# Optimization experiments

Hardware: AMD Instinct MI355X
Metric: run time of the kernel (lower is better)

The kernel has to match this reference:

```python
import jax, jax.numpy as jnp
import numpy as np

B, S, D, H = 4, 1024, 1024, 16
DK = D // H  # 64


def setup_inputs() -> dict:
    key = jax.random.key(0)
    kx, kq, kk, kv, ko = jax.random.split(key, 5)
    scale = 1.0 / np.sqrt(D)
    x = jax.random.normal(kx, (B, S, D), dtype=jnp.float32)
    # per-head torch nn.Linear weights stacked: [H, d_k, d_model]
    Wq = jax.random.uniform(kq, (H, DK, D), jnp.float32, -scale, scale)
    Wk = jax.random.uniform(kk, (H, DK, D), jnp.float32, -scale, scale)
    Wv = jax.random.uniform(kv, (H, DK, D), jnp.float32, -scale, scale)
    Wo = jax.random.uniform(ko, (D, D), jnp.float32, -scale, scale)  # torch layout [out, in]
    # causal mask, broadcastable to (B, H, S, S); True = keep
    mask = jnp.tril(jnp.ones((S, S), dtype=bool))[None, None]
    return {"x": x, "Wq": Wq, "Wk": Wk, "Wv": Wv, "Wo": Wo, "mask": mask}


def reference(x, Wq, Wk, Wv, Wo, mask):
    # self-attention: context = x. Batched equivalent of the per-head loop.
    Q = jnp.einsum('bsd,hkd->bhsk', x, Wq)  # (B,H,S,DK)
    K = jnp.einsum('bsd,hkd->bhsk', x, Wk)
    V = jnp.einsum('bsd,hkd->bhsk', x, Wv)
    scores = jnp.einsum('bhqd,bhkd->bhqk', Q, K) / jnp.sqrt(jnp.float32(DK))
    scores = jnp.where(mask, scores, jnp.float32(-jnp.inf))
    weights = jax.nn.softmax(scores, axis=-1)  # (B,H,S,S)
    out = jnp.einsum('bhqk,bhkd->bhqd', weights, V)  # (B,H,S,DK)
    # concat heads along feature dim (head order preserved), then W_o
    concat = jnp.swapaxes(out, 1, 2).reshape(B, S, D)
    output = jnp.einsum('bqd,od->bqo', concat, Wo)
    return output, weights
```

## Files before the change

kernel.cpp:

```cpp
#include <hip/hip_runtime.h>
#include <hip/hip_bf16.h>

#define BB 4
#define SS 1024
#define DD 1024
#define HH 16
#define DKK 64

typedef __bf16 bf16;
typedef __bf16 bf16x8 __attribute__((ext_vector_type(8)));
typedef __bf16 bf16x4 __attribute__((ext_vector_type(4)));
typedef float f32x4 __attribute__((ext_vector_type(4)));

#define MFMA(a, b, c) __builtin_amdgcn_mfma_f32_16x16x32_bf16((a), (b), (c), 0, 0, 0)

__device__ __forceinline__ bf16x8 load8(const bf16* p) {
    return *reinterpret_cast<const bf16x8*>(p);
}

__device__ __forceinline__ void gload16(const bf16* g, bf16* l) {
    __builtin_amdgcn_global_load_lds(
        (const __attribute__((address_space(1))) void*)g,
        (__attribute__((address_space(3))) void*)l, 16, 0, 0);
}

__global__ __launch_bounds__(256) void cvt_bf16(const float* __restrict__ x,
                                                const float* __restrict__ Wq,
                                                const float* __restrict__ Wk,
                                                const float* __restrict__ Wv,
                                                const float* __restrict__ Wo,
                                                bf16* __restrict__ dst) {
    const size_t MEG = 1024 * 1024;
    size_t e = ((size_t)blockIdx.x * 256 + threadIdx.x) * 4;
    const float* src;
    size_t off;
    if (e < 4 * MEG)      { src = x;  off = e; }
    else if (e < 5 * MEG) { src = Wq; off = e - 4 * MEG; }
    else if (e < 6 * MEG) { src = Wk; off = e - 5 * MEG; }
    else if (e < 7 * MEG) { src = Wv; off = e - 6 * MEG; }
    else                  { src = Wo; off = e - 7 * MEG; }
    f32x4 v = *reinterpret_cast<const f32x4*>(src + off);
    bf16x4 o;
    o[0] = (bf16)v[0]; o[1] = (bf16)v[1]; o[2] = (bf16)v[2]; o[3] = (bf16)v[3];
    *reinterpret_cast<bf16x4*>(dst + e) = o;
}

template <int MODE>
__global__ __launch_bounds__(256) void gemm128(const bf16* __restrict__ A,
                                               const bf16* __restrict__ Bm,
                                               void* __restrict__ o0,
                                               void* __restrict__ o1,
                                               void* __restrict__ o2,
                                               float* __restrict__ Wgt) {
    const int lane = threadIdx.x & 63;
    const int wave = threadIdx.x >> 6;
    const int wr = wave >> 1, wc = wave & 1;
    const int m0 = blockIdx.x * 128;
    const int n0 = blockIdx.y * 128;
    const int K = DD;

    __shared__ __align__(16) bf16 As[128][32];
    __shared__ __align__(16) bf16 Bs[128][32];

    const int r0 = wave * 32 + (lane >> 2);
    const int r1 = r0 + 16;
    const int csw = ((lane & 3) ^ (r0 & 3)) * 8;

    const bf16* Ag0 = A + (size_t)(m0 + r0) * K + csw;
    const bf16* Ag1 = A + (size_t)(m0 + r1) * K + csw;
    const bf16* Bg0 = Bm + (size_t)(n0 + r0) * K + csw;
    const bf16* Bg1 = Bm + (size_t)(n0 + r1) * K + csw;
    bf16* Aw0 = &As[wave * 32][0];
    bf16* Aw1 = &As[wave * 32 + 16][0];
    bf16* Bw0 = &Bs[wave * 32][0];
    bf16* Bw1 = &Bs[wave * 32 + 16][0];

    const int rsw = ((lane >> 4) ^ (lane & 3)) * 8;
    const int rrow = lane & 15;

    f32x4 acc[4][4] = {};

    for (int k0 = 0; k0 < K; k0 += 32) {
        __syncthreads();
        gload16(Ag0 + k0, Aw0);
        gload16(Ag1 + k0, Aw1);
        gload16(Bg0 + k0, Bw0);
        gload16(Bg1 + k0, Bw1);
        __syncthreads();
        bf16x8 af[4], bfr[4];
#pragma unroll
        for (int i = 0; i < 4; i++)
            af[i] = *reinterpret_cast<const bf16x8*>(&As[wr * 64 + i * 16 + rrow][rsw]);
#pragma unroll
        for (int j = 0; j < 4; j++)
            bfr[j] = *reinterpret_cast<const bf16x8*>(&Bs[wc * 64 + j * 16 + rrow][rsw]);
#pragma unroll
        for (int i = 0; i < 4; i++)
#pragma unroll
            for (int j = 0; j < 4; j++)
                acc[i][j] = MFMA(af[i], bfr[j], acc[i][j]);
    }

    if constexpr (MODE == 0) {
        bf16* Qo = (bf16*)o0;
        bf16* Ko = (bf16*)o1;
        bf16* Vto = (bf16*)o2;
        const int z = n0 >> 10;
#pragma unroll
        for (int i = 0; i < 4; i++)
#pragma unroll
            for (int j = 0; j < 4; j++)
#pragma unroll
                for (int r = 0; r < 4; r++) {
                    int m = m0 + wr * 64 + i * 16 + (lane >> 4) * 4 + r;
                    int n = n0 + wc * 64 + j * 16 + (lane & 15);
                    int b = m >> 10, s = m & 1023;
                    int nn = n & 1023, h = nn >> 6, dk = nn & 63;
                    bf16 v = (bf16)acc[i][j][r];
                    if (z == 0)
                        Qo[(((size_t)(b * HH + h)) * SS + s) * DKK + dk] = v;
                    else if (z == 1)
                        Ko[(((size_t)(b * HH + h)) * SS + s) * DKK + dk] = v;
                    else
                        Vto[(((size_t)(b * HH + h)) * DKK + dk) * SS + s] = v;
                }
        const int bid = blockIdx.y * 32 + blockIdx.x;
        const int zrow = threadIdx.x >> 2;
        const int zcl = threadIdx.x & 3;
        const f32x4 z4 = {0.f, 0.f, 0.f, 0.f};
        for (int band = bid; band < 1024; band += 768) {
            const int bh = band >> 4, qb = band & 15;
            const int c0 = (qb + 1) * 64;
            const int nc4 = (1024 - c0) >> 2;
            if (nc4 <= 0) continue;
            float* rp = Wgt + ((size_t)bh * SS + qb * 64 + zrow) * SS + c0;
            for (int c = zcl; c < nc4; c += 4)
                *reinterpret_cast<f32x4*>(rp + c * 4) = z4;
        }
    } else {
        float* Out = (float*)o0;
#pragma unroll
        for (int i = 0; i < 4; i++)
#pragma unroll
            for (int j = 0; j < 4; j++)
#pragma unroll
                for (int r = 0; r < 4; r++) {
                    int m = m0 + wr * 64 + i * 16 + (lane >> 4) * 4 + r;
                    int n = n0 + wc * 64 + j * 16 + (lane & 15);
                    Out[(size_t)m * DD + n] = acc[i][j][r];
                }
    }
}

__global__ __launch_bounds__(256, 4) void attn(const bf16* __restrict__ Q,
                                               const bf16* __restrict__ K,
                                               const bf16* __restrict__ Vt,
                                               float* __restrict__ Wgt,
                                               bf16* __restrict__ Ctx) {
    const int tid = threadIdx.x;
    const int lane = tid & 63;
    const int wave = tid >> 6;
    const int bh = blockIdx.x;
    const int qb = (blockIdx.y + (blockIdx.x & 3)) & 15;
    const int q0 = qb * 64 + wave * 16;
    const int lr = lane & 15;
    const int g = lane >> 4;
    const int lk8 = g * 8;
    const int rbase = g * 4;
    const int own_diag = q0 >> 4;
    const int nch = qb + 1;

    const bf16* Qb = Q + (size_t)bh * SS * DKK;
    const bf16* Kb = K + (size_t)bh * SS * DKK;
    const bf16* Vb = Vt + (size_t)bh * DKK * SS;
    float* Wrow = Wgt + ((size_t)bh * SS + q0) * SS;

    __shared__ __align__(16) bf16 Ks[2][64][64];
    __shared__ __align__(16) bf16 Vs[2][64][64];
    __shared__ __align__(16) bf16 Ps[4][16][40];

    const int skr = tid >> 2;
    const int sc0 = tid & 3;
    const int sw0 = (sc0 ^ (skr & 7)) * 8;
    const int sw1 = ((sc0 + 4) ^ (skr & 7)) * 8;

    bf16x8 qa0 = load8(Qb + (size_t)(q0 + lr) * DKK + lk8);
    bf16x8 qa1 = load8(Qb + (size_t)(q0 + lr) * DKK + 32 + lk8);
#pragma unroll
    for (int i = 0; i < 8; i++) {
        qa0[i] = (bf16)((float)qa0[i] * 0.125f);
        qa1[i] = (bf16)((float)qa1[i] * 0.125f);
    }

    const int rsw0 = (g ^ (lr & 7)) * 8;
    const int rsw1 = ((4 + g) ^ (lr & 7)) * 8;

    float sl[4] = {0.f, 0.f, 0.f, 0.f};

    {
        bf16x8 ka = load8(Kb + (size_t)skr * DKK + sc0 * 8);
        bf16x8 kb_ = load8(Kb + (size_t)skr * DKK + (sc0 + 4) * 8);
        *reinterpret_cast<bf16x8*>(&Ks[0][skr][sw0]) = ka;
        *reinterpret_cast<bf16x8*>(&Ks[0][skr][sw1]) = kb_;
        __syncthreads();
        for (int ch = 0; ch < nch; ch++) {
            const int cur = ch & 1;
            if (ch + 1 < nch) {
                ka = load8(Kb + (size_t)((ch + 1) * 64 + skr) * DKK + sc0 * 8);
                kb_ = load8(Kb + (size_t)((ch + 1) * 64 + skr) * DKK + (sc0 + 4) * 8);
            }
#pragma unroll
            for (int t = 0; t < 4; t++) {
                const int kt = ch * 4 + t;
                if (kt <= own_diag) {
                    bf16x8 kb0 = *reinterpret_cast<const bf16x8*>(&Ks[cur][t * 16 + lr][rsw0]);
                    bf16x8 kb1 = *reinterpret_cast<const bf16x8*>(&Ks[cur][t * 16 + lr][rsw1]);
                    f32x4 sc = {};
                    sc = MFMA(qa0, kb0, sc);
                    sc = MFMA(qa1, kb1, sc);
                    const int kcol = kt * 16 + lr;
#pragma unroll
                    for (int r = 0; r < 4; r++)
                        sl[r] += (kcol <= q0 + rbase + r) ? __expf(sc[r]) : 0.f;
                }
            }
            if (ch + 1 < nch) {
                *reinterpret_cast<bf16x8*>(&Ks[cur ^ 1][skr][sw0]) = ka;
                *reinterpret_cast<bf16x8*>(&Ks[cur ^ 1][skr][sw1]) = kb_;
            }
            __syncthreads();
        }
    }
    float inv[4];
#pragma unroll
    for (int r = 0; r < 4; r++) {
        float t = sl[r];
        t += __shfl_xor(t, 1);
        t += __shfl_xor(t, 2);
        t += __shfl_xor(t, 4);
        t += __shfl_xor(t, 8);
        inv[r] = 1.f / t;
    }

    f32x4 oacc[4] = {};
    {
        bf16x8 ka = load8(Kb + (size_t)skr * DKK + sc0 * 8);
        bf16x8 kb_ = load8(Kb + (size_t)skr * DKK + (sc0 + 4) * 8);
        bf16x8 va = load8(Vb + (size_t)skr * SS + sc0 * 8);
        bf16x8 vb_ = load8(Vb + (size_t)skr * SS + (sc0 + 4) * 8);
        *reinterpret_cast<bf16x8*>(&Ks[0][skr][sw0]) = ka;
        *reinterpret_cast<bf16x8*>(&Ks[0][skr][sw1]) = kb_;
        *reinterpret_cast<bf16x8*>(&Vs[0][skr][sw0]) = va;
        *reinterpret_cast<bf16x8*>(&Vs[0][skr][sw1]) = vb_;
        __syncthreads();
        for (int ch = 0; ch < nch; ch++) {
            const int cur = ch & 1;
            if (ch + 1 < nch) {
                ka = load8(Kb + (size_t)((ch + 1) * 64 + skr) * DKK + sc0 * 8);
                kb_ = load8(Kb + (size_t)((ch + 1) * 64 + skr) * DKK + (sc0 + 4) * 8);
                va = load8(Vb + (size_t)skr * SS + (ch + 1) * 64 + sc0 * 8);
                vb_ = load8(Vb + (size_t)skr * SS + (ch + 1) * 64 + (sc0 + 4) * 8);
            }
#pragma unroll
            for (int t = 0; t < 4; t++) {
                const int kt = ch * 4 + t;
                if (kt <= own_diag) {
                    bf16x8 kb0 = *reinterpret_cast<const bf16x8*>(&Ks[cur][t * 16 + lr][rsw0]);
                    bf16x8 kb1 = *reinterpret_cast<const bf16x8*>(&Ks[cur][t * 16 + lr][rsw1]);
                    f32x4 sc = {};
                    sc = MFMA(qa0, kb0, sc);
                    sc = MFMA(qa1, kb1, sc);
                    const int kcol = kt * 16 + lr;
#pragma unroll
                    for (int r = 0; r < 4; r++) {
                        float p = (kcol <= q0 + rbase + r) ? __expf(sc[r]) * inv[r] : 0.f;
                        Ps[wave][rbase + r][(t & 1) * 16 + lr] = (bf16)p;
                    }
                } else {
#pragma unroll
                    for (int r = 0; r < 4; r++)
                        Ps[wave][rbase + r][(t & 1) * 16 + lr] = (bf16)0.f;
                }
                if (t & 1) {
                    const int colbase = ch * 64 + (t >> 1) * 32;
                    const int prow = lane >> 2;
                    const int pcol = (lane & 3) * 8;
                    bf16x8 pv8 = *reinterpret_cast<const bf16x8*>(&Ps[wave][prow][pcol]);
                    f32x4 w0, w1;
#pragma unroll
                    for (int i = 0; i < 4; i++) {
                        w0[i] = (float)pv8[i];
                        w1[i] = (float)pv8[4 + i];
                    }
                    float* dst = Wrow + (size_t)prow * SS + colbase + pcol;
                    *reinterpret_cast<f32x4*>(dst) = w0;
                    *reinterpret_cast<f32x4*>(dst + 4) = w1;
                    if (kt - 1 <= own_diag) {
                        const int p2 = t >> 1;
                        bf16x8 pf = *reinterpret_cast<const bf16x8*>(&Ps[wave][lr][lk8]);
#pragma unroll
                        for (int j = 0; j < 4; j++) {
                            bf16x8 vb = *reinterpret_cast<const bf16x8*>(
                                &Vs[cur][j * 16 + lr][((4 * p2 + g) ^ (lr & 7)) * 8]);
                            oacc[j] = MFMA(pf, vb, oacc[j]);
                        }
                    }
                }
            }
            if (ch + 1 < nch) {
                *reinterpret_cast<bf16x8*>(&Ks[cur ^ 1][skr][sw0]) = ka;
                *reinterpret_cast<bf16x8*>(&Ks[cur ^ 1][skr][sw1]) = kb_;
                *reinterpret_cast<bf16x8*>(&Vs[cur ^ 1][skr][sw0]) = va;
                *reinterpret_cast<bf16x8*>(&Vs[cur ^ 1][skr][sw1]) = vb_;
            }
            __syncthreads();
        }
    }

    const int b = bh >> 4, h = bh & 15;
#pragma unroll
    for (int j = 0; j < 4; j++)
#pragma unroll
        for (int r = 0; r < 4; r++) {
            int qrow = q0 + rbase + r;
            int col = h * 64 + j * 16 + lr;
            Ctx[((size_t)b * SS + qrow) * DD + col] = (bf16)oacc[j][r];
        }
}

extern "C" void kernel_launch(void* const* d_in, const int* in_sizes, int n_in,
                              void* d_out, int out_size, void* d_ws, size_t ws_size,
                              hipStream_t stream) {
    const float* x  = (const float*)d_in[0];
    const float* Wq = (const float*)d_in[1];
    const float* Wk = (const float*)d_in[2];
    const float* Wv = (const float*)d_in[3];
    const float* Wo = (const float*)d_in[4];

    float* out = (float*)d_out;
    float* wgt = out + (size_t)BB * SS * DD;

    const size_t MEG = 1024 * 1024;
    bf16* xb   = (bf16*)d_ws;
    bf16* wcat = xb + 4 * MEG;
    bf16* wob  = xb + 7 * MEG;
    bf16* qws  = xb + 8 * MEG;
    bf16* kws  = xb + 12 * MEG;
    bf16* vws  = xb + 16 * MEG;
    bf16* cws  = xb + 20 * MEG;

    cvt_bf16<<<dim3(8192), 256, 0, stream>>>(x, Wq, Wk, Wv, Wo, xb);
    gemm128<0><<<dim3(32, 24), 256, 0, stream>>>(xb, wcat, qws, kws, vws, wgt);
    attn<<<dim3(64, 16), 256, 0, stream>>>(qws, kws, vws, wgt, cws);
    gemm128<1><<<dim3(32, 8), 256, 0, stream>>>(cws, wob, out, nullptr, nullptr,
                                                nullptr);
}
```

Measured before the change: 147.2 us.

## Use 64x64 tiles for output projection GEMM and raise wave priority around MFMAs

The output projection GEMM becomes its own kernel with 64x64 tiles and a 64x16 grid (1024 blocks) instead of 128x128 tiles on a 32x8 grid (256 blocks). This should fill the CUs much better on a 256-CU part. The cost is less reuse per block and more LDS and global traffic. The attention kernel also wraps its MFMA sequences in s_setprio(1)/s_setprio(0), so waves issuing matrix ops get scheduling priority over waves doing softmax and stores.

```diff
diff --git a/kernel.cpp b/kernel.cpp
--- a/kernel.cpp
+++ b/kernel.cpp
@@ -45,13 +45,12 @@
     *reinterpret_cast<bf16x4*>(dst + e) = o;
 }
 
-template <int MODE>
-__global__ __launch_bounds__(256) void gemm128(const bf16* __restrict__ A,
-                                               const bf16* __restrict__ Bm,
-                                               void* __restrict__ o0,
-                                               void* __restrict__ o1,
-                                               void* __restrict__ o2,
-                                               float* __restrict__ Wgt) {
+__global__ __launch_bounds__(256) void gemm_qkv(const bf16* __restrict__ A,
+                                                const bf16* __restrict__ Bm,
+                                                bf16* __restrict__ Qo,
+                                                bf16* __restrict__ Ko,
+                                                bf16* __restrict__ Vto,
+                                                float* __restrict__ Wgt) {
     const int lane = threadIdx.x & 63;
     const int wave = threadIdx.x >> 6;
     const int wr = wave >> 1, wc = wave & 1;
@@ -101,55 +100,94 @@
                 acc[i][j] = MFMA(af[i], bfr[j], acc[i][j]);
     }
 
-    if constexpr (MODE == 0) {
-        bf16* Qo = (bf16*)o0;
-        bf16* Ko = (bf16*)o1;
-        bf16* Vto = (bf16*)o2;
-        const int z = n0 >> 10;
-#pragma unroll
-        for (int i = 0; i < 4; i++)
-#pragma unroll
-            for (int j = 0; j < 4; j++)
-#pragma unroll
-                for (int r = 0; r < 4; r++) {
-                    int m = m0 + wr * 64 + i * 16 + (lane >> 4) * 4 + r;
-                    int n = n0 + wc * 64 + j * 16 + (lane & 15);
-                    int b = m >> 10, s = m & 1023;
-                    int nn = n & 1023, h = nn >> 6, dk = nn & 63;
-                    bf16 v = (bf16)acc[i][j][r];
-                    if (z == 0)
-                        Qo[(((size_t)(b * HH + h)) * SS + s) * DKK + dk] = v;
-                    else if (z == 1)
-                        Ko[(((size_t)(b * HH + h)) * SS + s) * DKK + dk] = v;
-                    else
-                        Vto[(((size_t)(b * HH + h)) * DKK + dk) * SS + s] = v;
-                }
-        const int bid = blockIdx.y * 32 + blockIdx.x;
-        const int zrow = threadIdx.x >> 2;
-        const int zcl = threadIdx.x & 3;
-        const f32x4 z4 = {0.f, 0.f, 0.f, 0.f};
-        for (int band = bid; band < 1024; band += 768) {
-            const int bh = band >> 4, qb = band & 15;
-            const int c0 = (qb + 1) * 64;
-            const int nc4 = (1024 - c0) >> 2;
-            if (nc4 <= 0) continue;
-            float* rp = Wgt + ((size_t)bh * SS + qb * 64 + zrow) * SS + c0;
-            for (int c = zcl; c < nc4; c += 4)
-                *reinterpret_cast<f32x4*>(rp + c * 4) = z4;
-        }
-    } else {
-        float* Out = (float*)o0;
-#pragma unroll
-        for (int i = 0; i < 4; i++)
-#pragma unroll
-            for (int j = 0; j < 4; j++)
-#pragma unroll
-                for (int r = 0; r < 4; r++) {
-                    int m = m0 + wr * 64 + i * 16 + (lane >> 4) * 4 + r;
-                    int n = n0 + wc * 64 + j * 16 + (lane & 15);
-                    Out[(size_t)m * DD + n] = acc[i][j][r];
-                }
-    }
+    const int z = n0 >> 10;
+#pragma unroll
+    for (int i = 0; i < 4; i++)
+#pragma unroll
+        for (int j = 0; j < 4; j++)
+#pragma unroll
+            for (int r = 0; r < 4; r++) {
+                int m = m0 + wr * 64 + i * 16 + (lane >> 4) * 4 + r;
+                int n = n0 + wc * 64 + j * 16 + (lane & 15);
+                int b = m >> 10, s = m & 1023;
+                int nn = n & 1023, h = nn >> 6, dk = nn & 63;
+                bf16 v = (bf16)acc[i][j][r];
+                if (z == 0)
+                    Qo[(((size_t)(b * HH + h)) * SS + s) * DKK + dk] = v;
+                else if (z == 1)
+                    Ko[(((size_t)(b * HH + h)) * SS + s) * DKK + dk] = v;
+                else
+                    Vto[(((size_t)(b * HH + h)) * DKK + dk) * SS + s] = v;
+            }
+    const int bid = blockIdx.y * 32 + blockIdx.x;
+    const int zrow = threadIdx.x >> 2;
+    const int zcl = threadIdx.x & 3;
+    const f32x4 z4 = {0.f, 0.f, 0.f, 0.f};
+    for (int band = bid; band < 1024; band += 768) {
+        const int bh = band >> 4, qb = band & 15;
+        const int c0 = (qb + 1) * 64;
+        const int nc4 = (1024 - c0) >> 2;
+        if (nc4 <= 0) continue;
+        float* rp = Wgt + ((size_t)bh * SS + qb * 64 + zrow) * SS + c0;
+        for (int c = zcl; c < nc4; c += 4)
+            *reinterpret_cast<f32x4*>(rp + c * 4) = z4;
+    }
+}
+
+__global__ __launch_bounds__(256) void gemm_out(const bf16* __restrict__ A,
+                                                const bf16* __restrict__ Bm,
+                                                float* __restrict__ Out) {
+    const int lane = threadIdx.x & 63;
+    const int wave = threadIdx.x >> 6;
+    const int wr = wave >> 1, wc = wave & 1;
+    const int m0 = blockIdx.x * 64;
+    const int n0 = blockIdx.y * 64;
+    const int K = DD;
+
+    __shared__ __align__(16) bf16 As[64][32];
+    __shared__ __align__(16) bf16 Bs[64][32];
+
+    const int srow = wave * 16 + (lane >> 2);
+    const int csw = ((lane & 3) ^ (srow & 3)) * 8;
+    const bf16* Ag = A + (size_t)(m0 + srow) * K + csw;
+    const bf16* Bg = Bm + (size_t)(n0 + srow) * K + csw;
+    bf16* Aw = &As[wave * 16][0];
+    bf16* Bw = &Bs[wave * 16][0];
+
+    const int rsw = ((lane >> 4) ^ (lane & 3)) * 8;
+    const int rrow = lane & 15;
+
+    f32x4 acc[2][2] = {};
+
+    for (int k0 = 0; k0 < K; k0 += 32) {
+        __syncthreads();
+        gload16(Ag + k0, Aw);
+        gload16(Bg + k0, Bw);
+        __syncthreads();
+        bf16x8 af[2], bfr[2];
+#pragma unroll
+        for (int i = 0; i < 2; i++)
+            af[i] = *reinterpret_cast<const bf16x8*>(&As[wr * 32 + i * 16 + rrow][rsw]);
+#pragma unroll
+        for (int j = 0; j < 2; j++)
+            bfr[j] = *reinterpret_cast<const bf16x8*>(&Bs[wc * 32 + j * 16 + rrow][rsw]);
+#pragma unroll
+        for (int i = 0; i < 2; i++)
+#pragma unroll
+            for (int j = 0; j < 2; j++)
+                acc[i][j] = MFMA(af[i], bfr[j], acc[i][j]);
+    }
+
+#pragma unroll
+    for (int i = 0; i < 2; i++)
+#pragma unroll
+        for (int j = 0; j < 2; j++)
+#pragma unroll
+            for (int r = 0; r < 4; r++) {
+                int m = m0 + wr * 32 + i * 16 + (lane >> 4) * 4 + r;
+                int n = n0 + wc * 32 + j * 16 + (lane & 15);
+                Out[(size_t)m * DD + n] = acc[i][j][r];
+            }
 }
 
 __global__ __launch_bounds__(256, 4) void attn(const bf16* __restrict__ Q,
@@ -215,9 +253,11 @@
                 if (kt <= own_diag) {
                     bf16x8 kb0 = *reinterpret_cast<const bf16x8*>(&Ks[cur][t * 16 + lr][rsw0]);
                     bf16x8 kb1 = *reinterpret_cast<const bf16x8*>(&Ks[cur][t * 16 + lr][rsw1]);
+                    __builtin_amdgcn_s_setprio(1);
                     f32x4 sc = {};
                     sc = MFMA(qa0, kb0, sc);
                     sc = MFMA(qa1, kb1, sc);
+                    __builtin_amdgcn_s_setprio(0);
                     const int kcol = kt * 16 + lr;
 #pragma unroll
                     for (int r = 0; r < 4; r++)
@@ -267,9 +307,11 @@
                 if (kt <= own_diag) {
                     bf16x8 kb0 = *reinterpret_cast<const bf16x8*>(&Ks[cur][t * 16 + lr][rsw0]);
                     bf16x8 kb1 = *reinterpret_cast<const bf16x8*>(&Ks[cur][t * 16 + lr][rsw1]);
+                    __builtin_amdgcn_s_setprio(1);
                     f32x4 sc = {};
                     sc = MFMA(qa0, kb0, sc);
                     sc = MFMA(qa1, kb1, sc);
+                    __builtin_amdgcn_s_setprio(0);
                     const int kcol = kt * 16 + lr;
 #pragma unroll
                     for (int r = 0; r < 4; r++) {
@@ -298,12 +340,14 @@
                     if (kt - 1 <= own_diag) {
                         const int p2 = t >> 1;
                         bf16x8 pf = *reinterpret_cast<const bf16x8*>(&Ps[wave][lr][lk8]);
+                        __builtin_amdgcn_s_setprio(1);
 #pragma unroll
                         for (int j = 0; j < 4; j++) {
                             bf16x8 vb = *reinterpret_cast<const bf16x8*>(
                                 &Vs[cur][j * 16 + lr][((4 * p2 + g) ^ (lr & 7)) * 8]);
                             oacc[j] = MFMA(pf, vb, oacc[j]);
                         }
+                        __builtin_amdgcn_s_setprio(0);
                     }
                 }
             }
@@ -350,8 +394,7 @@
     bf16* cws  = xb + 20 * MEG;
 
     cvt_bf16<<<dim3(8192), 256, 0, stream>>>(x, Wq, Wk, Wv, Wo, xb);
-    gemm128<0><<<dim3(32, 24), 256, 0, stream>>>(xb, wcat, qws, kws, vws, wgt);
+    gemm_qkv<<<dim3(32, 24), 256, 0, stream>>>(xb, wcat, qws, kws, vws, wgt);
     attn<<<dim3(64, 16), 256, 0, stream>>>(qws, kws, vws, wgt, cws);
-    gemm128<1><<<dim3(32, 8), 256, 0, stream>>>(cws, wob, out, nullptr, nullptr,
-                                                nullptr);
-}
+    gemm_out<<<dim3(64, 16), 256, 0, stream>>>(cws, wob, out);
+}
```

After: 144.4 us (median of 2 runs). Within noise of the previous version (-1.9%).
